# Kernel optimization log

Measured on AMD Instinct MI355X. Metric: run time of the kernel, lower is better.

## Reference

```python
import jax, jax.numpy as jnp
import numpy as np

N_NODES = 30000


def gcn_conv(x, src, dst, ew, W, b, n):
    # x: [N, Fin] -> linear first (PyG GCNConv), then normalized scatter-add
    h = x @ W  # [N, Fout]
    loops = jnp.arange(n, dtype=src.dtype)
    s = jnp.concatenate([src, loops])
    d = jnp.concatenate([dst, loops])
    w = jnp.concatenate([ew, jnp.ones((n,), dtype=ew.dtype)])
    deg = jax.ops.segment_sum(w, d, num_segments=n)
    dinv = jnp.where(deg > 0, jax.lax.rsqrt(jnp.where(deg > 0, deg, 1.0)), 0.0)
    norm = dinv[s] * w * dinv[d]  # [E+N]
    msg = h[s] * norm[:, None]  # [E+N, Fout]
    out = jax.ops.segment_sum(msg, d, num_segments=n)
    return out + b


def setup_inputs() -> dict:
    key = jax.random.key(0)
    ks = jax.random.split(key, 16)
    n, e, f, c = N_NODES, 480000, 64, 64
    dims = [f, 2 * c, 4 * c, 8 * c]  # 64 -> 128 -> 256 -> 512
    num_classes = 40

    def lin(k, fi, fo):
        k1, k2 = jax.random.split(k)
        s = 1.0 / np.sqrt(fi)
        return (jax.random.uniform(k1, (fi, fo), jnp.float32, -s, s),
                jax.random.uniform(k2, (fo,), jnp.float32, -s, s))

    W1, b1 = lin(ks[0], dims[0], dims[1])
    W2, b2 = lin(ks[1], dims[1], dims[2])
    W3, b3 = lin(ks[2], dims[2], dims[3])
    fW1, fb1 = lin(ks[3], dims[3], dims[3])
    fW2, fb2 = lin(ks[4], dims[3], num_classes)
    return {
        "x": jax.random.normal(ks[5], (n, f), jnp.float32),
        "edge_index": jax.random.randint(ks[6], (2, e), 0, n, jnp.int32),
        "edge_attr": jax.random.uniform(ks[7], (e, 1), jnp.float32),
        "W1": W1, "b1": b1, "W2": W2, "b2": b2, "W3": W3, "b3": b3,
        "fW1": fW1, "fb1": fb1, "fW2": fW2, "fb2": fb2,
    }


def reference(x, edge_index, edge_attr, W1, b1, W2, b2, W3, b3, fW1, fb1, fW2, fb2):
    n = x.shape[0]
    src, dst = edge_index[0], edge_index[1]
    ew = edge_attr.squeeze(-1)
    h = jax.nn.relu(gcn_conv(x, src, dst, ew, W1, b1, n))
    h = jax.nn.relu(gcn_conv(h, src, dst, ew, W2, b2, n))
    h = jax.nn.relu(gcn_conv(h, src, dst, ew, W3, b3, n))
    h = jax.nn.relu(h @ fW1 + fb1)
    h = h @ fW2 + fb2
    return jax.nn.log_softmax(h, axis=1)
```

## Files before the change

kernel.cpp:

```cpp
#include <hip/hip_runtime.h>
#include <cstdint>
#include <cstddef>


typedef _Float16 f16;
typedef _Float16 half8 __attribute__((ext_vector_type(8)));
typedef _Float16 half4 __attribute__((ext_vector_type(4)));
typedef float v4f __attribute__((ext_vector_type(4)));
typedef unsigned long long u64;

__device__ inline void gload_lds16(const void* g, void* l) {
    __builtin_amdgcn_global_load_lds(
        (const __attribute__((address_space(1))) unsigned int*)g,
        (__attribute__((address_space(3))) unsigned int*)l, 16, 0, 0);
}


__global__ __launch_bounds__(256) void k_edge1(const int* __restrict__ dst, const float* __restrict__ ew,
                                               u64* __restrict__ packed, int* __restrict__ eslot, int E) {
    int t = blockIdx.x * blockDim.x + threadIdx.x;
    int e0 = t * 4;
    if (e0 + 3 < E) {
        int4 d4 = *(const int4*)(dst + e0);
        float4 w4 = *(const float4*)(ew + e0);
        u64 a0 = ((u64)__float2uint_rn(w4.x * 1048576.f) << 24) | 1ULL;
        u64 a1 = ((u64)__float2uint_rn(w4.y * 1048576.f) << 24) | 1ULL;
        u64 a2 = ((u64)__float2uint_rn(w4.z * 1048576.f) << 24) | 1ULL;
        u64 a3 = ((u64)__float2uint_rn(w4.w * 1048576.f) << 24) | 1ULL;
        u64 o0 = atomicAdd(&packed[d4.x], a0);
        u64 o1 = atomicAdd(&packed[d4.y], a1);
        u64 o2 = atomicAdd(&packed[d4.z], a2);
        u64 o3 = atomicAdd(&packed[d4.w], a3);
        int4 s;
        s.x = (int)(o0 & 0xFFFFFF); s.y = (int)(o1 & 0xFFFFFF);
        s.z = (int)(o2 & 0xFFFFFF); s.w = (int)(o3 & 0xFFFFFF);
        *(int4*)(eslot + e0) = s;
    } else {
        for (int e = e0; e < E; ++e) {
            u64 a = ((u64)__float2uint_rn(ew[e] * 1048576.f) << 24) | 1ULL;
            u64 o = atomicAdd(&packed[dst[e]], a);
            eslot[e] = (int)(o & 0xFFFFFF);
        }
    }
}

__global__ __launch_bounds__(256) void k_dinv_scan1(const u64* __restrict__ packed,
                                                    float* __restrict__ dinv, int* __restrict__ cnt,
                                                    int* __restrict__ bsum, int n) {
    int i = blockIdx.x * 256 + threadIdx.x;
    int c = 0;
    if (i < n) {
        u64 pk = packed[i];
        c = (int)(pk & 0xFFFFFF);
        float d = 1.0f + (float)(pk >> 24) * (1.0f / 1048576.f);
        float r = rsqrtf(d);
        r = r * (1.5f - 0.5f * d * r * r);
        dinv[i] = r;
        cnt[i] = c;
    }
    int v = c;
#pragma unroll
    for (int o = 32; o; o >>= 1) v += __shfl_xor(v, o);
    __shared__ int s[4];
    if ((threadIdx.x & 63) == 0) s[threadIdx.x >> 6] = v;
    __syncthreads();
    if (threadIdx.x == 0) bsum[blockIdx.x] = s[0] + s[1] + s[2] + s[3];
}

__device__ inline int block_scan_incl(int v) {
    __shared__ int ws[4];
    int lane = threadIdx.x & 63, w = threadIdx.x >> 6;
#pragma unroll
    for (int off = 1; off < 64; off <<= 1) {
        int t = __shfl_up(v, off);
        if (lane >= off) v += t;
    }
    if (lane == 63) ws[w] = v;
    __syncthreads();
    int add = 0;
#pragma unroll
    for (int i = 0; i < 4; ++i) add += (i < w) ? ws[i] : 0;
    __syncthreads();
    return v + add;
}

__global__ __launch_bounds__(256) void k_scan2(const int* __restrict__ bsum, int* __restrict__ boff, int nb) {
    __shared__ int carry;
    if (threadIdx.x == 0) carry = 0;
    __syncthreads();
    for (int base = 0; base < nb; base += 256) {
        int i = base + threadIdx.x;
        int v = (i < nb) ? bsum[i] : 0;
        int incl = block_scan_incl(v);
        int c = carry;
        if (i < nb) boff[i] = c + incl - v;
        __syncthreads();
        if (threadIdx.x == 255) carry = c + incl;
        __syncthreads();
    }
}

__global__ __launch_bounds__(256) void k_scan3(const int* __restrict__ cnt, const int* __restrict__ boff,
                                               int* __restrict__ rowptr, int n) {
    int i = blockIdx.x * 256 + threadIdx.x;
    int v = (i < n) ? cnt[i] : 0;
    int incl = block_scan_incl(v);
    if (i < n) rowptr[i] = boff[blockIdx.x] + incl - v;
    if (i == n - 1) rowptr[n] = boff[blockIdx.x] + incl;
}

__global__ __launch_bounds__(256) void k_fill(const int* __restrict__ src, const int* __restrict__ dst,
                                              const float* __restrict__ ew, const int* __restrict__ eslot,
                                              const float* __restrict__ dinv, const int* __restrict__ rowptr,
                                              int* __restrict__ csr_src, float* __restrict__ csr_norm, int E) {
    int e = blockIdx.x * blockDim.x + threadIdx.x;
    if (e < E) {
        int d = dst[e], s = src[e];
        int idx = rowptr[d] + eslot[e];
        csr_src[idx] = s;
        csr_norm[idx] = dinv[s] * ew[e] * dinv[d];
    }
}

struct PrepArgs {
    u64* packed; int n;
    const float* x; f16* xh; int xt4;
    const float* W[5]; f16* WT[5];
    int lgK[5]; int N[5]; int off[6];
};
__global__ __launch_bounds__(256) void k_prep(PrepArgs a) {
    int i = blockIdx.x * 256 + threadIdx.x;
    if (i < a.n) { a.packed[i] = 0ULL; return; }
    int j = i - a.n;
    if (j < a.xt4) {
        float4 v = *(const float4*)(a.x + (size_t)j * 4);
        half4 h = {(f16)v.x, (f16)v.y, (f16)v.z, (f16)v.w};
        *(half4*)(a.xh + (size_t)j * 4) = h;
        return;
    }
    int w = j - a.xt4;
#pragma unroll
    for (int s = 0; s < 5; ++s) {
        if (w >= a.off[s] && w < a.off[s + 1]) {
            int li = w - a.off[s];
            int K = 1 << a.lgK[s];
            int nr = li >> a.lgK[s], k = li & (K - 1);
            float v = (nr < a.N[s]) ? a.W[s][(size_t)k * a.N[s] + nr] : 0.f;
            a.WT[s][li] = (f16)v;
        }
    }
}

template <int F>
__global__ __launch_bounds__(256) void k_agg(const f16* __restrict__ h,
                                             const float* __restrict__ dinv, const int* __restrict__ rowptr,
                                             const int* __restrict__ csr_src, const float* __restrict__ csr_norm,
                                             f16* __restrict__ o, int n) {
    constexpr int LPN = F / 8;
    constexpr int NPW = 64 / LPN;
    int wave = (int)((blockIdx.x * (unsigned)blockDim.x + threadIdx.x) >> 6);
    int lane = threadIdx.x & 63;
    int grp = lane / LPN, lin = lane % LPN;
    int node = wave * NPW + grp;
    if (node >= n) return;
    float di = dinv[node], w0 = di * di;
    float acc[8];
#pragma unroll
    for (int i = 0; i < 8; ++i) acc[i] = 0.f;

    auto gat = [&](int s, float w) {
        half8 x = *(const half8*)(h + (size_t)s * F + lin * 8);
#pragma unroll
        for (int i = 0; i < 8; ++i) acc[i] += w * (float)x[i];
    };

    gat(node, w0);
    int beg = rowptr[node], end = rowptr[node + 1];
    int j = beg;
    for (; j + 3 < end; j += 4) {
        int s0 = csr_src[j], s1 = csr_src[j + 1], s2 = csr_src[j + 2], s3 = csr_src[j + 3];
        float u0 = csr_norm[j], u1 = csr_norm[j + 1], u2 = csr_norm[j + 2], u3 = csr_norm[j + 3];
        gat(s0, u0); gat(s1, u1); gat(s2, u2); gat(s3, u3);
    }
    for (; j < end; ++j) gat(csr_src[j], csr_norm[j]);

    half8 v;
#pragma unroll
    for (int i = 0; i < 8; ++i) v[i] = (f16)acc[i];
    *(half8*)(o + (size_t)node * F + (size_t)lin * 8) = v;
}

template <bool RELU>
__global__ __launch_bounds__(256) void k_mm(const f16* __restrict__ A, const f16* __restrict__ BT,
                                            const float* __restrict__ bias, f16* __restrict__ Ch,
                                            int M, int N, int K, int nB, int nwg) {
    __shared__ f16 lsA[2][128 * 64];
    __shared__ f16 lsB[2][128 * 64];
    int wg = blockIdx.x;
    int q = nwg >> 3, r = nwg & 7;
    int xcd = wg & 7, lin = wg >> 3;
    int wgs = (xcd < r) ? (xcd * (q + 1) + lin) : (r * (q + 1) + (xcd - r) * q + lin);
    int bm = wgs / nB, bn = wgs % nB;

    int tid = threadIdx.x;
    int lane = tid & 63, wid = tid >> 6;
    int l16 = lane & 15, lhi = lane >> 4;
    int wm = (wid >> 1) * 64, wn = (wid & 1) * 64;
    int brow = bm * 128, bcol = bn * 128;

    v4f acc[4][4] = {};

    auto stageA = [&](int buf, int k0) {
#pragma unroll
        for (int it = 0; it < 4; ++it) {
            int b = it * 4096 + tid * 16;
            int row = b >> 7;
            int s = ((b >> 4) & 7) ^ (row & 7);
            gload_lds16(A + (size_t)(brow + row) * K + k0 + s * 8, ((char*)&lsA[buf][0]) + b);
        }
    };
    auto stageB = [&](int buf, int k0) {
#pragma unroll
        for (int it = 0; it < 4; ++it) {
            int b = it * 4096 + tid * 16;
            int row = b >> 7;
            int s = ((b >> 4) & 7) ^ (row & 7);
            gload_lds16(BT + (size_t)(bcol + row) * K + k0 + s * 8, ((char*)&lsB[buf][0]) + b);
        }
    };

    int nk = K >> 6;
    stageA(0, 0);
    stageB(0, 0);
    for (int kt = 0; kt < nk; ++kt) {
        int cur = kt & 1;
        __syncthreads();
        if (kt + 1 < nk) { stageA(cur ^ 1, (kt + 1) << 6); stageB(cur ^ 1, (kt + 1) << 6); }
#pragma unroll
        for (int ks = 0; ks < 2; ++ks) {
            half8 bf[4];
#pragma unroll
            for (int fn = 0; fn < 4; ++fn) {
                int row = wn + fn * 16 + l16;
                int sidx = (ks * 4 + lhi) ^ (row & 7);
                bf[fn] = *(const half8*)(&lsB[cur][0] + row * 64 + sidx * 8);
            }
#pragma unroll
            for (int fm = 0; fm < 4; ++fm) {
                int row = wm + fm * 16 + l16;
                int sidx = (ks * 4 + lhi) ^ (row & 7);
                half8 af = *(const half8*)(&lsA[cur][0] + row * 64 + sidx * 8);
#pragma unroll
                for (int fn = 0; fn < 4; ++fn)
                    acc[fm][fn] = __builtin_amdgcn_mfma_f32_16x16x32_f16(bf[fn], af, acc[fm][fn], 0, 0, 0);
            }
        }
    }
#pragma unroll
    for (int fm = 0; fm < 4; ++fm) {
        int m = brow + wm + fm * 16 + l16;
        if (m >= M) continue;
#pragma unroll
        for (int fn = 0; fn < 4; ++fn) {
            int nb = bcol + wn + fn * 16 + lhi * 4;
            v4f bv = *(const v4f*)(bias + nb);
            v4f v = acc[fm][fn] + bv;
            if (RELU) {
#pragma unroll
                for (int rr = 0; rr < 4; ++rr) v[rr] = fmaxf(v[rr], 0.f);
            }
            half4 hv = {(f16)v[0], (f16)v[1], (f16)v[2], (f16)v[3]};
            *(half4*)(Ch + (size_t)m * N + nb) = hv;
        }
    }
}

template <bool RELU>
__global__ __launch_bounds__(512, 2) void k_mm8(const f16* __restrict__ A, const f16* __restrict__ BT,
                                                const float* __restrict__ bias, f16* __restrict__ Ch,
                                                int M, int N, int K, int nB, int nwg) {
    __shared__ f16 lsA[2][256 * 64];
    __shared__ f16 lsB[2][256 * 64];
    int wg = blockIdx.x;
    int q = nwg >> 3, r = nwg & 7;
    int xcd = wg & 7, lin = wg >> 3;
    int wgs = (xcd < r) ? (xcd * (q + 1) + lin) : (r * (q + 1) + (xcd - r) * q + lin);
    int bm = wgs / nB, bn = wgs % nB;

    int tid = threadIdx.x;
    int lane = tid & 63, wid = tid >> 6;
    int l16 = lane & 15, lhi = lane >> 4;
    int wm = (wid >> 2) * 128, wn = (wid & 3) * 64;
    int brow = bm * 256, bcol = bn * 256;

    v4f acc[8][4] = {};

    auto stageA = [&](int buf, int k0) {
#pragma unroll
        for (int it = 0; it < 4; ++it) {
            int b = it * 8192 + tid * 16;
            int row = b >> 7;
            int s = ((b >> 4) & 7) ^ (row & 7);
            gload_lds16(A + (size_t)(brow + row) * K + k0 + s * 8, ((char*)&lsA[buf][0]) + b);
        }
    };
    auto stageB = [&](int buf, int k0) {
#pragma unroll
        for (int it = 0; it < 4; ++it) {
            int b = it * 8192 + tid * 16;
            int row = b >> 7;
            int s = ((b >> 4) & 7) ^ (row & 7);
            gload_lds16(BT + (size_t)(bcol + row) * K + k0 + s * 8, ((char*)&lsB[buf][0]) + b);
        }
    };

    int nk = K >> 6;
    stageA(0, 0);
    stageB(0, 0);
    for (int kt = 0; kt < nk; ++kt) {
        int cur = kt & 1;
        __syncthreads();
        if (kt + 1 < nk) { stageA(cur ^ 1, (kt + 1) << 6); stageB(cur ^ 1, (kt + 1) << 6); }
#pragma unroll
        for (int ks = 0; ks < 2; ++ks) {
            half8 bf[4];
#pragma unroll
            for (int fn = 0; fn < 4; ++fn) {
                int row = wn + fn * 16 + l16;
                int sidx = (ks * 4 + lhi) ^ (row & 7);
                bf[fn] = *(const half8*)(&lsB[cur][0] + row * 64 + sidx * 8);
            }
#pragma unroll
            for (int fm = 0; fm < 8; ++fm) {
                int row = wm + fm * 16 + l16;
                int sidx = (ks * 4 + lhi) ^ (row & 7);
                half8 af = *(const half8*)(&lsA[cur][0] + row * 64 + sidx * 8);
#pragma unroll
                for (int fn = 0; fn < 4; ++fn)
                    acc[fm][fn] = __builtin_amdgcn_mfma_f32_16x16x32_f16(bf[fn], af, acc[fm][fn], 0, 0, 0);
            }
        }
    }
#pragma unroll
    for (int fm = 0; fm < 8; ++fm) {
        int m = brow + wm + fm * 16 + l16;
        if (m >= M) continue;
#pragma unroll
        for (int fn = 0; fn < 4; ++fn) {
            int nb = bcol + wn + fn * 16 + lhi * 4;
            v4f bv = *(const v4f*)(bias + nb);
            v4f v = acc[fm][fn] + bv;
            if (RELU) {
#pragma unroll
                for (int rr = 0; rr < 4; ++rr) v[rr] = fmaxf(v[rr], 0.f);
            }
            half4 hv = {(f16)v[0], (f16)v[1], (f16)v[2], (f16)v[3]};
            *(half4*)(Ch + (size_t)m * N + nb) = hv;
        }
    }
}

__global__ __launch_bounds__(256) void k_mmfc2(const f16* __restrict__ A, const f16* __restrict__ BT,
                                               const float* __restrict__ bias, float* __restrict__ out,
                                               int M, int K) {
    __shared__ f16 lsA[2][256 * 64];
    __shared__ f16 lsB[2][64 * 64];
    int bm = blockIdx.x;
    int tid = threadIdx.x;
    int lane = tid & 63, wid = tid >> 6;
    int l16 = lane & 15, lhi = lane >> 4;
    int wm = wid * 64;
    int brow = bm * 256;

    v4f acc[4][4] = {};

    auto stageA = [&](int buf, int k0) {
#pragma unroll
        for (int it = 0; it < 8; ++it) {
            int b = it * 4096 + tid * 16;
            int row = b >> 7;
            int s = ((b >> 4) & 7) ^ (row & 7);
            gload_lds16(A + (size_t)(brow + row) * K + k0 + s * 8, ((char*)&lsA[buf][0]) + b);
        }
    };
    auto stageB = [&](int buf, int k0) {
#pragma unroll
        for (int it = 0; it < 2; ++it) {
            int b = it * 4096 + tid * 16;
            int row = b >> 7;
            int s = ((b >> 4) & 7) ^ (row & 7);
            gload_lds16(BT + (size_t)row * K + k0 + s * 8, ((char*)&lsB[buf][0]) + b);
        }
    };

    int nk = K >> 6;
    stageA(0, 0);
    stageB(0, 0);
    for (int kt = 0; kt < nk; ++kt) {
        int cur = kt & 1;
        __syncthreads();
        if (kt + 1 < nk) { stageA(cur ^ 1, (kt + 1) << 6); stageB(cur ^ 1, (kt + 1) << 6); }
#pragma unroll
        for (int ks = 0; ks < 2; ++ks) {
            half8 bf[4];
#pragma unroll
            for (int fn = 0; fn < 4; ++fn) {
                int row = fn * 16 + l16;
                int sidx = (ks * 4 + lhi) ^ (row & 7);
                bf[fn] = *(const half8*)(&lsB[cur][0] + row * 64 + sidx * 8);
            }
#pragma unroll
            for (int fm = 0; fm < 4; ++fm) {
                int row = wm + fm * 16 + l16;
                int sidx = (ks * 4 + lhi) ^ (row & 7);
                half8 af = *(const half8*)(&lsA[cur][0] + row * 64 + sidx * 8);
#pragma unroll
                for (int fn = 0; fn < 4; ++fn)
                    acc[fm][fn] = __builtin_amdgcn_mfma_f32_16x16x32_f16(bf[fn], af, acc[fm][fn], 0, 0, 0);
            }
        }
    }

    float bv[4][4];
#pragma unroll
    for (int fn = 0; fn < 4; ++fn)
#pragma unroll
        for (int rr = 0; rr < 4; ++rr) {
            int nn = fn * 16 + lhi * 4 + rr;
            bv[fn][rr] = (nn < 40) ? bias[nn] : 0.f;
        }

#pragma unroll
    for (int fm = 0; fm < 4; ++fm) {
        int m = brow + wm + fm * 16 + l16;
        float v[4][4];
        float mx = -INFINITY;
#pragma unroll
        for (int fn = 0; fn < 4; ++fn)
#pragma unroll
            for (int rr = 0; rr < 4; ++rr) {
                int nn = fn * 16 + lhi * 4 + rr;
                v[fn][rr] = acc[fm][fn][rr] + bv[fn][rr];
                if (nn < 40) mx = fmaxf(mx, v[fn][rr]);
            }
        mx = fmaxf(mx, __shfl_xor(mx, 16));
        mx = fmaxf(mx, __shfl_xor(mx, 32));
        float s = 0.f;
#pragma unroll
        for (int fn = 0; fn < 3; ++fn)
#pragma unroll
            for (int rr = 0; rr < 4; ++rr) {
                int nn = fn * 16 + lhi * 4 + rr;
                if (nn < 40) s += __expf(v[fn][rr] - mx);
            }
        s += __shfl_xor(s, 16);
        s += __shfl_xor(s, 32);
        float ls = __logf(s);
        if (m < M) {
#pragma unroll
            for (int fn = 0; fn < 3; ++fn)
#pragma unroll
                for (int rr = 0; rr < 4; ++rr) {
                    int nn = fn * 16 + lhi * 4 + rr;
                    if (nn < 40) out[(size_t)m * 40 + nn] = v[fn][rr] - mx - ls;
                }
        }
    }
}


extern "C" void kernel_launch(void* const* d_in, const int* in_sizes, int n_in,
                              void* d_out, int out_size, void* d_ws, size_t ws_size,
                              hipStream_t stream) {
    const float* x   = (const float*)d_in[0];
    const int*   ei  = (const int*)d_in[1];
    const float* ea  = (const float*)d_in[2];
    const float* W1  = (const float*)d_in[3];  const float* b1  = (const float*)d_in[4];
    const float* W2  = (const float*)d_in[5];  const float* b2  = (const float*)d_in[6];
    const float* W3  = (const float*)d_in[7];  const float* b3  = (const float*)d_in[8];
    const float* fW1 = (const float*)d_in[9];  const float* fb1 = (const float*)d_in[10];
    const float* fW2 = (const float*)d_in[11]; const float* fb2 = (const float*)d_in[12];

    int n = in_sizes[0] / 64;
    int E = in_sizes[1] / 2;
    int Mpad = ((n + 255) / 256) * 256;
    const int* src = ei;
    const int* dst = ei + E;
    float* out = (float*)d_out;

    char* p = (char*)d_ws;
    auto alloc = [&](size_t bytes) -> char* {
        char* r = p;
        p += (bytes + 255) & ~(size_t)255;
        return r;
    };
    int nb256 = (n + 255) / 256;
    u64*   packed   = (u64*)alloc((size_t)n * 8);
    float* dinv     = (float*)alloc((size_t)n * 4);
    int*   cnt      = (int*)alloc((size_t)n * 4);
    int*   rowptr   = (int*)alloc((size_t)(n + 1) * 4);
    int*   bsum     = (int*)alloc((size_t)nb256 * 4);
    int*   boff     = (int*)alloc((size_t)nb256 * 4);
    int*   eslot    = (int*)alloc((size_t)E * 4);
    int*   csr_src  = (int*)alloc((size_t)E * 4);
    float* csr_norm = (float*)alloc((size_t)E * 4);
    f16* XH  = (f16*)alloc((size_t)Mpad * 64 * 2);
    f16* W1T = (f16*)alloc((size_t)128 * 64 * 2);
    f16* W2T = (f16*)alloc((size_t)256 * 128 * 2);
    f16* W3T = (f16*)alloc((size_t)512 * 256 * 2);
    f16* F1T = (f16*)alloc((size_t)512 * 512 * 2);
    f16* F2T = (f16*)alloc((size_t)64 * 512 * 2);
    f16* AGG = (f16*)alloc((size_t)Mpad * 256 * 2);
    f16* HA  = (f16*)alloc((size_t)Mpad * 512 * 2);
    f16* HB  = (f16*)alloc((size_t)Mpad * 512 * 2);

    const int tb = 256;
    int eB = (E + tb - 1) / tb;
    int e4B = (E / 4 + tb - 1) / tb + 1;
    auto aggB = [&](int npw) {
        long waves = (n + npw - 1) / npw;
        return (int)((waves * 64 + tb - 1) / tb);
    };

    {
        PrepArgs a;
        a.packed = packed; a.n = n;
        a.x = x; a.xh = XH; a.xt4 = n * 16;
        a.W[0] = W1;  a.WT[0] = W1T; a.lgK[0] = 6; a.N[0] = 128;
        a.W[1] = W2;  a.WT[1] = W2T; a.lgK[1] = 7; a.N[1] = 256;
        a.W[2] = W3;  a.WT[2] = W3T; a.lgK[2] = 8; a.N[2] = 512;
        a.W[3] = fW1; a.WT[3] = F1T; a.lgK[3] = 9; a.N[3] = 512;
        a.W[4] = fW2; a.WT[4] = F2T; a.lgK[4] = 9; a.N[4] = 40;
        a.off[0] = 0;
        a.off[1] = a.off[0] + 128 * 64;
        a.off[2] = a.off[1] + 256 * 128;
        a.off[3] = a.off[2] + 512 * 256;
        a.off[4] = a.off[3] + 512 * 512;
        a.off[5] = a.off[4] + 64 * 512;
        int tot = a.n + a.xt4 + a.off[5];
        k_prep<<<(tot + tb - 1) / tb, tb, 0, stream>>>(a);
    }

    k_edge1<<<e4B, tb, 0, stream>>>(dst, ea, packed, eslot, E);
    k_dinv_scan1<<<nb256, tb, 0, stream>>>(packed, dinv, cnt, bsum, n);
    k_scan2<<<1, tb, 0, stream>>>(bsum, boff, nb256);
    k_scan3<<<nb256, tb, 0, stream>>>(cnt, boff, rowptr, n);
    k_fill<<<eB, tb, 0, stream>>>(src, dst, ea, eslot, dinv, rowptr, csr_src, csr_norm, E);

    auto mm8 = [&](const f16* a, const f16* bt, const float* bias, f16* ch, int N, int K) {
        int nB2 = N / 256;
        int nwg = (Mpad / 256) * nB2;
        k_mm8<true><<<nwg, 512, 0, stream>>>(a, bt, bias, ch, n, N, K, nB2, nwg);
    };

    k_agg<64><<<aggB(8), tb, 0, stream>>>(XH, dinv, rowptr, csr_src, csr_norm, AGG, n);
    {
        int nwg = Mpad / 128;
        k_mm<true><<<nwg, 256, 0, stream>>>(AGG, W1T, b1, HA, n, 128, 64, 1, nwg);
    }
    k_agg<128><<<aggB(4), tb, 0, stream>>>(HA, dinv, rowptr, csr_src, csr_norm, AGG, n);
    mm8(AGG, W2T, b2, HB, 256, 128);
    k_agg<256><<<aggB(2), tb, 0, stream>>>(HB, dinv, rowptr, csr_src, csr_norm, AGG, n);
    mm8(AGG, W3T, b3, HA, 512, 256);
    mm8(HA, F1T, fb1, HB, 512, 512);
    k_mmfc2<<<Mpad / 256, 256, 0, stream>>>(HB, F2T, fb2, out, n, 512);
}
```

Measured before the change: 206.0 us.

## Replicate degree counters, fuse scan into decoupled-lookback kernel, dual-accumulate aggregation

Spreads each node's packed degree/count atomic across four replicated slots chosen by thread index, which cuts atomic contention on hot destinations. The three scan kernels are merged into one single-pass scan in which each block publishes its total through a flag array and sums the totals of earlier blocks, and k_fill adds a per-replica base offset. The aggregation loop is unrolled to 8 neighbours with two independent accumulators for more loads in flight. The costs are four times the counter memory, an extra rbase array, and a cross-block spin-wait that relies on earlier blocks being scheduled first.

```diff
diff --git a/kernel.cpp b/kernel.cpp
--- a/kernel.cpp
+++ b/kernel.cpp
@@ -17,9 +17,10 @@
 
 
 __global__ __launch_bounds__(256) void k_edge1(const int* __restrict__ dst, const float* __restrict__ ew,
-                                               u64* __restrict__ packed, int* __restrict__ eslot, int E) {
+                                               u64* __restrict__ packed4, int* __restrict__ eslot, int E) {
     int t = blockIdx.x * blockDim.x + threadIdx.x;
     int e0 = t * 4;
+    int r = t & 3;
     if (e0 + 3 < E) {
         int4 d4 = *(const int4*)(dst + e0);
         float4 w4 = *(const float4*)(ew + e0);
@@ -27,10 +28,10 @@
         u64 a1 = ((u64)__float2uint_rn(w4.y * 1048576.f) << 24) | 1ULL;
         u64 a2 = ((u64)__float2uint_rn(w4.z * 1048576.f) << 24) | 1ULL;
         u64 a3 = ((u64)__float2uint_rn(w4.w * 1048576.f) << 24) | 1ULL;
-        u64 o0 = atomicAdd(&packed[d4.x], a0);
-        u64 o1 = atomicAdd(&packed[d4.y], a1);
-        u64 o2 = atomicAdd(&packed[d4.z], a2);
-        u64 o3 = atomicAdd(&packed[d4.w], a3);
+        u64 o0 = atomicAdd(&packed4[(size_t)d4.x * 4 + r], a0);
+        u64 o1 = atomicAdd(&packed4[(size_t)d4.y * 4 + r], a1);
+        u64 o2 = atomicAdd(&packed4[(size_t)d4.z * 4 + r], a2);
+        u64 o3 = atomicAdd(&packed4[(size_t)d4.w * 4 + r], a3);
         int4 s;
         s.x = (int)(o0 & 0xFFFFFF); s.y = (int)(o1 & 0xFFFFFF);
         s.z = (int)(o2 & 0xFFFFFF); s.w = (int)(o3 & 0xFFFFFF);
@@ -38,33 +39,10 @@
     } else {
         for (int e = e0; e < E; ++e) {
             u64 a = ((u64)__float2uint_rn(ew[e] * 1048576.f) << 24) | 1ULL;
-            u64 o = atomicAdd(&packed[dst[e]], a);
+            u64 o = atomicAdd(&packed4[(size_t)dst[e] * 4 + r], a);
             eslot[e] = (int)(o & 0xFFFFFF);
         }
     }
-}
-
-__global__ __launch_bounds__(256) void k_dinv_scan1(const u64* __restrict__ packed,
-                                                    float* __restrict__ dinv, int* __restrict__ cnt,
-                                                    int* __restrict__ bsum, int n) {
-    int i = blockIdx.x * 256 + threadIdx.x;
-    int c = 0;
-    if (i < n) {
-        u64 pk = packed[i];
-        c = (int)(pk & 0xFFFFFF);
-        float d = 1.0f + (float)(pk >> 24) * (1.0f / 1048576.f);
-        float r = rsqrtf(d);
-        r = r * (1.5f - 0.5f * d * r * r);
-        dinv[i] = r;
-        cnt[i] = c;
-    }
-    int v = c;
-#pragma unroll
-    for (int o = 32; o; o >>= 1) v += __shfl_xor(v, o);
-    __shared__ int s[4];
-    if ((threadIdx.x & 63) == 0) s[threadIdx.x >> 6] = v;
-    __syncthreads();
-    if (threadIdx.x == 0) bsum[blockIdx.x] = s[0] + s[1] + s[2] + s[3];
 }
 
 __device__ inline int block_scan_incl(int v) {
@@ -84,54 +62,82 @@
     return v + add;
 }
 
-__global__ __launch_bounds__(256) void k_scan2(const int* __restrict__ bsum, int* __restrict__ boff, int nb) {
-    __shared__ int carry;
-    if (threadIdx.x == 0) carry = 0;
+__global__ __launch_bounds__(256) void k_graph(const u64* __restrict__ packed4,
+                                               float* __restrict__ dinv, int4* __restrict__ rbase,
+                                               int* __restrict__ rowptr, unsigned* __restrict__ gflag,
+                                               int n, int E) {
+    int blk = blockIdx.x, tid = threadIdx.x;
+    int i = blk * 256 + tid;
+    int cnt = 0;
+    if (i < n) {
+        const u64* pp = packed4 + (size_t)i * 4;
+        u64 p0 = pp[0], p1 = pp[1], p2 = pp[2], p3 = pp[3];
+        int c0 = (int)(p0 & 0xFFFFFF), c1 = (int)(p1 & 0xFFFFFF);
+        int c2 = (int)(p2 & 0xFFFFFF), c3 = (int)(p3 & 0xFFFFFF);
+        cnt = c0 + c1 + c2 + c3;
+        rbase[i] = make_int4(0, c0, c0 + c1, c0 + c1 + c2);
+        float d = 1.0f + (float)((p0 >> 24) + (p1 >> 24) + (p2 >> 24) + (p3 >> 24)) * (1.0f / 1048576.f);
+        float rq = rsqrtf(d);
+        rq = rq * (1.5f - 0.5f * d * rq * rq);
+        dinv[i] = rq;
+    }
+    int incl = block_scan_incl(cnt);
+    __shared__ int stot;
+    if (tid == 255) stot = incl;
     __syncthreads();
-    for (int base = 0; base < nb; base += 256) {
-        int i = base + threadIdx.x;
-        int v = (i < nb) ? bsum[i] : 0;
-        int incl = block_scan_incl(v);
-        int c = carry;
-        if (i < nb) boff[i] = c + incl - v;
-        __syncthreads();
-        if (threadIdx.x == 255) carry = c + incl;
-        __syncthreads();
-    }
-}
-
-__global__ __launch_bounds__(256) void k_scan3(const int* __restrict__ cnt, const int* __restrict__ boff,
-                                               int* __restrict__ rowptr, int n) {
-    int i = blockIdx.x * 256 + threadIdx.x;
-    int v = (i < n) ? cnt[i] : 0;
-    int incl = block_scan_incl(v);
-    if (i < n) rowptr[i] = boff[blockIdx.x] + incl - v;
-    if (i == n - 1) rowptr[n] = boff[blockIdx.x] + incl;
+    if (tid == 0)
+        __hip_atomic_store(&gflag[blk], (unsigned)stot | 0x80000000u,
+                           __ATOMIC_RELEASE, __HIP_MEMORY_SCOPE_AGENT);
+    __shared__ int sprefix;
+    if (tid == 0) sprefix = 0;
+    __syncthreads();
+    if (tid < 64) {
+        int pref = 0;
+        for (int j = tid; j < blk; j += 64) {
+            unsigned v;
+            do {
+                v = __hip_atomic_load(&gflag[j], __ATOMIC_ACQUIRE, __HIP_MEMORY_SCOPE_AGENT);
+            } while (!(v & 0x80000000u));
+            pref += (int)(v & 0x7FFFFFFFu);
+        }
+#pragma unroll
+        for (int o = 32; o; o >>= 1) pref += __shfl_xor(pref, o);
+        if (tid == 0) sprefix = pref;
+    }
+    __syncthreads();
+    if (i < n) rowptr[i] = sprefix + incl - cnt;
+    if (blk == 0 && tid == 0) rowptr[n] = E;
 }
 
 __global__ __launch_bounds__(256) void k_fill(const int* __restrict__ src, const int* __restrict__ dst,
                                               const float* __restrict__ ew, const int* __restrict__ eslot,
                                               const float* __restrict__ dinv, const int* __restrict__ rowptr,
+                                              const int4* __restrict__ rbase,
                                               int* __restrict__ csr_src, float* __restrict__ csr_norm, int E) {
     int e = blockIdx.x * blockDim.x + threadIdx.x;
     if (e < E) {
         int d = dst[e], s = src[e];
-        int idx = rowptr[d] + eslot[e];
+        int r = (e >> 2) & 3;
+        const int* rb = (const int*)&rbase[d];
+        int idx = rowptr[d] + rb[r] + eslot[e];
         csr_src[idx] = s;
         csr_norm[idx] = dinv[s] * ew[e] * dinv[d];
     }
 }
 
 struct PrepArgs {
-    u64* packed; int n;
+    u64* packed4; int n4;
+    unsigned* gflag; int nbf;
     const float* x; f16* xh; int xt4;
     const float* W[5]; f16* WT[5];
     int lgK[5]; int N[5]; int off[6];
 };
 __global__ __launch_bounds__(256) void k_prep(PrepArgs a) {
     int i = blockIdx.x * 256 + threadIdx.x;
-    if (i < a.n) { a.packed[i] = 0ULL; return; }
-    int j = i - a.n;
+    if (i < a.n4) { a.packed4[i] = 0ULL; return; }
+    int g = i - a.n4;
+    if (g < a.nbf) { a.gflag[g] = 0u; return; }
+    int j = g - a.nbf;
     if (j < a.xt4) {
         float4 v = *(const float4*)(a.x + (size_t)j * 4);
         half4 h = {(f16)v.x, (f16)v.y, (f16)v.z, (f16)v.w};
@@ -164,29 +170,37 @@
     int node = wave * NPW + grp;
     if (node >= n) return;
     float di = dinv[node], w0 = di * di;
-    float acc[8];
-#pragma unroll
-    for (int i = 0; i < 8; ++i) acc[i] = 0.f;
-
-    auto gat = [&](int s, float w) {
+    float acca[8], accb[8];
+#pragma unroll
+    for (int i = 0; i < 8; ++i) { acca[i] = 0.f; accb[i] = 0.f; }
+
+    auto gat = [&](float* acc, int s, float w) {
         half8 x = *(const half8*)(h + (size_t)s * F + lin * 8);
 #pragma unroll
         for (int i = 0; i < 8; ++i) acc[i] += w * (float)x[i];
     };
 
-    gat(node, w0);
+    gat(acca, node, w0);
     int beg = rowptr[node], end = rowptr[node + 1];
     int j = beg;
-    for (; j + 3 < end; j += 4) {
+    for (; j + 7 < end; j += 8) {
         int s0 = csr_src[j], s1 = csr_src[j + 1], s2 = csr_src[j + 2], s3 = csr_src[j + 3];
+        int s4 = csr_src[j + 4], s5 = csr_src[j + 5], s6 = csr_src[j + 6], s7 = csr_src[j + 7];
         float u0 = csr_norm[j], u1 = csr_norm[j + 1], u2 = csr_norm[j + 2], u3 = csr_norm[j + 3];
-        gat(s0, u0); gat(s1, u1); gat(s2, u2); gat(s3, u3);
-    }
-    for (; j < end; ++j) gat(csr_src[j], csr_norm[j]);
+        float u4 = csr_norm[j + 4], u5 = csr_norm[j + 5], u6 = csr_norm[j + 6], u7 = csr_norm[j + 7];
+        gat(acca, s0, u0); gat(accb, s1, u1); gat(acca, s2, u2); gat(accb, s3, u3);
+        gat(acca, s4, u4); gat(accb, s5, u5); gat(acca, s6, u6); gat(accb, s7, u7);
+    }
+    for (; j + 1 < end; j += 2) {
+        int s0 = csr_src[j], s1 = csr_src[j + 1];
+        float u0 = csr_norm[j], u1 = csr_norm[j + 1];
+        gat(acca, s0, u0); gat(accb, s1, u1);
+    }
+    if (j < end) gat(acca, csr_src[j], csr_norm[j]);
 
     half8 v;
 #pragma unroll
-    for (int i = 0; i < 8; ++i) v[i] = (f16)acc[i];
+    for (int i = 0; i < 8; ++i) v[i] = (f16)(acca[i] + accb[i]);
     *(half8*)(o + (size_t)node * F + (size_t)lin * 8) = v;
 }
 
@@ -495,12 +509,11 @@
         return r;
     };
     int nb256 = (n + 255) / 256;
-    u64*   packed   = (u64*)alloc((size_t)n * 8);
+    u64*   packed4  = (u64*)alloc((size_t)n * 4 * 8);
+    unsigned* gflag = (unsigned*)alloc((size_t)nb256 * 4);
     float* dinv     = (float*)alloc((size_t)n * 4);
-    int*   cnt      = (int*)alloc((size_t)n * 4);
+    int4*  rbase    = (int4*)alloc((size_t)n * 16);
     int*   rowptr   = (int*)alloc((size_t)(n + 1) * 4);
-    int*   bsum     = (int*)alloc((size_t)nb256 * 4);
-    int*   boff     = (int*)alloc((size_t)nb256 * 4);
     int*   eslot    = (int*)alloc((size_t)E * 4);
     int*   csr_src  = (int*)alloc((size_t)E * 4);
     float* csr_norm = (float*)alloc((size_t)E * 4);
@@ -524,7 +537,8 @@
 
     {
         PrepArgs a;
-        a.packed = packed; a.n = n;
+        a.packed4 = packed4; a.n4 = n * 4;
+        a.gflag = gflag; a.nbf = nb256;
         a.x = x; a.xh = XH; a.xt4 = n * 16;
         a.W[0] = W1;  a.WT[0] = W1T; a.lgK[0] = 6; a.N[0] = 128;
         a.W[1] = W2;  a.WT[1] = W2T; a.lgK[1] = 7; a.N[1] = 256;
@@ -537,15 +551,13 @@
         a.off[3] = a.off[2] + 512 * 256;
         a.off[4] = a.off[3] + 512 * 512;
         a.off[5] = a.off[4] + 64 * 512;
-        int tot = a.n + a.xt4 + a.off[5];
+        int tot = a.n4 + a.nbf + a.xt4 + a.off[5];
         k_prep<<<(tot + tb - 1) / tb, tb, 0, stream>>>(a);
     }
 
-    k_edge1<<<e4B, tb, 0, stream>>>(dst, ea, packed, eslot, E);
-    k_dinv_scan1<<<nb256, tb, 0, stream>>>(packed, dinv, cnt, bsum, n);
-    k_scan2<<<1, tb, 0, stream>>>(bsum, boff, nb256);
-    k_scan3<<<nb256, tb, 0, stream>>>(cnt, boff, rowptr, n);
-    k_fill<<<eB, tb, 0, stream>>>(src, dst, ea, eslot, dinv, rowptr, csr_src, csr_norm, E);
+    k_edge1<<<e4B, tb, 0, stream>>>(dst, ea, packed4, eslot, E);
+    k_graph<<<nb256, tb, 0, stream>>>(packed4, dinv, rbase, rowptr, gflag, n, E);
+    k_fill<<<eB, tb, 0, stream>>>(src, dst, ea, eslot, dinv, rowptr, rbase, csr_src, csr_norm, E);
 
     auto mm8 = [&](const f16* a, const f16* bt, const float* bias, f16* ch, int N, int K) {
         int nB2 = N / 256;
```

After: 214.4 us. 1.04x slower.
